# Kernel tuning notes

Measured on AMD Instinct MI355X. Metric: run time of the kernel, lower is better.

## Reference

```python
import jax, jax.numpy as jnp
import numpy as np

NEG_SLOPE = 0.2


def _gat_layer(x, W, a_src, a_dst, b, src, dst, n_nodes, heads, dim):
    # x: [N, F_in]; W: [F_in, heads*dim]
    h = (x @ W).reshape(n_nodes, heads, dim)            # [N,H,D]
    e_src = (h * a_src).sum(-1)                          # [N,H]
    e_dst = (h * a_dst).sum(-1)                          # [N,H]
    e = jax.nn.leaky_relu(e_src[src] + e_dst[dst], NEG_SLOPE)  # [E,H]
    # edge softmax over incoming edges of each target node
    m = jax.ops.segment_max(e, dst, num_segments=n_nodes)      # [N,H]
    ex = jnp.exp(e - m[dst])
    denom = jax.ops.segment_sum(ex, dst, num_segments=n_nodes)  # [N,H]
    alpha = ex / denom[dst]                              # [E,H]
    out = jax.ops.segment_sum(h[src] * alpha[:, :, None], dst,
                              num_segments=n_nodes)      # [N,H,D]
    return out.reshape(n_nodes, heads * dim) + b


def setup_inputs() -> dict:
    key = jax.random.key(0)
    ks = jax.random.split(key, 10)
    N, E, F_in = 100000, 1600000, 300
    x = jax.random.normal(ks[0], (N, F_in), dtype=jnp.float32)
    edge_index = jax.random.randint(ks[1], (2, E), 0, N, dtype=jnp.int64)
    s = 0.1
    return {
        'x': x,
        'edge_index': edge_index,
        'W1': jax.random.normal(ks[2], (F_in, 64), jnp.float32) * s,
        'att_src1': jax.random.normal(ks[3], (8, 8), jnp.float32) * s,
        'att_dst1': jax.random.normal(ks[4], (8, 8), jnp.float32) * s,
        'b1': jax.random.normal(ks[5], (64,), jnp.float32) * s,
        'W2': jax.random.normal(ks[6], (64, 64), jnp.float32) * s,
        'att_src2': jax.random.normal(ks[7], (1, 64), jnp.float32) * s,
        'att_dst2': jax.random.normal(ks[8], (1, 64), jnp.float32) * s,
        'b2': jax.random.normal(ks[9], (64,), jnp.float32) * s,
    }


def reference(x, edge_index, W1, att_src1, att_dst1, b1, W2, att_src2, att_dst2, b2):
    N = x.shape[0]
    # add self-loops (PyG GATConv default)
    loop = jnp.arange(N, dtype=edge_index.dtype)
    src = jnp.concatenate([edge_index[0], loop])
    dst = jnp.concatenate([edge_index[1], loop])
    # dropout p=0.6 is identity in eval mode
    h = _gat_layer(x, W1, att_src1, att_dst1, b1, src, dst, N, 8, 8)    # [N,64]
    h = jax.nn.elu(h)
    h = _gat_layer(h, W2, att_src2, att_dst2, b2, src, dst, N, 1, 64)   # [N,64]
    return jax.nn.log_softmax(h, axis=1)
```

## Files before the change

### kernel.cpp

```cpp
#include <hip/hip_runtime.h>
#include <math.h>

using short8 = __attribute__((ext_vector_type(8))) short;
using f32x4  = __attribute__((ext_vector_type(4))) float;

#define NBLKS 512
#define BPAD  800

__device__ __forceinline__ unsigned short f2bf(float f) {
    unsigned u = __float_as_uint(f);
    unsigned r = u + 0x7FFF + ((u >> 16) & 1);
    return (unsigned short)(r >> 16);
}


__global__ void detect64_kernel(const int* __restrict__ ei, int E, int* __restrict__ flag) {
    __shared__ int any;
    if (threadIdx.x == 0) any = 0;
    __syncthreads();
    for (int i = threadIdx.x; i < 1024; i += 256) {
        if (ei[2 * i + 1] != 0) { any = 1; break; }
    }
    __syncthreads();
    if (threadIdx.x == 0) *flag = (any ? 0 : 1);
}


__global__ __launch_bounds__(256) void binA_kernel(
    const int* __restrict__ ei, int E, int N, const int* __restrict__ flag,
    int nbuck, int* __restrict__ hist, int chunk) {
    __shared__ int lh[BPAD];
    for (int i = threadIdx.x; i < nbuck; i += 256) lh[i] = 0;
    __syncthreads();
    int is64 = *flag;
    int Etot = E + N;
    int beg = blockIdx.x * chunk, end = min(Etot, beg + chunk);
    for (int i = beg + threadIdx.x; i < end; i += 256) {
        int d = (i < E) ? (is64 ? ei[2 * (E + i)] : ei[E + i]) : (i - E);
        atomicAdd(&lh[d >> 7], 1);
    }
    __syncthreads();
    for (int i = threadIdx.x; i < nbuck; i += 256) hist[blockIdx.x * BPAD + i] = lh[i];
}

__global__ void scanBlocks_kernel(int* __restrict__ hist, int nbuck, int* __restrict__ bucketTotal) {
    int bin = blockIdx.x * 256 + threadIdx.x;
    if (bin >= nbuck) return;
    int run = 0;
    for (int b = 0; b < NBLKS; b++) {
        int v = hist[b * BPAD + bin];
        hist[b * BPAD + bin] = run;
        run += v;
    }
    bucketTotal[bin] = run;
}

__global__ void scanBucket_kernel(const int* __restrict__ bucketTotal, int nbuck,
                                  int* __restrict__ bucketBase) {
    __shared__ int s[1024];
    int t = threadIdx.x;
    int v = (t < nbuck) ? bucketTotal[t] : 0;
    s[t] = v;
    __syncthreads();
    for (int off = 1; off < 1024; off <<= 1) {
        int x = (t >= off) ? s[t - off] : 0;
        __syncthreads();
        s[t] += x;
        __syncthreads();
    }
    if (t < nbuck) bucketBase[t] = s[t] - v;
    if (t == nbuck - 1) bucketBase[nbuck] = s[t];
}

__global__ __launch_bounds__(256) void binB_kernel(
    const int* __restrict__ ei, int E, int N, const int* __restrict__ flag,
    int nbuck, const int* __restrict__ hist, const int* __restrict__ bucketBase,
    int* __restrict__ tmp, int chunk) {
    __shared__ int cur[BPAD];
    for (int i = threadIdx.x; i < nbuck; i += 256)
        cur[i] = bucketBase[i] + hist[blockIdx.x * BPAD + i];
    __syncthreads();
    int is64 = *flag;
    int Etot = E + N;
    int beg = blockIdx.x * chunk, end = min(Etot, beg + chunk);
    for (int i = beg + threadIdx.x; i < end; i += 256) {
        int s, d;
        if (i < E) {
            if (is64) { s = ei[2 * i]; d = ei[2 * (E + i)]; }
            else      { s = ei[i];     d = ei[E + i]; }
        } else { s = i - E; d = i - E; }
        int pos = atomicAdd(&cur[d >> 7], 1);
        tmp[pos] = ((d & 127) << 17) | s;
    }
}

__global__ __launch_bounds__(256) void binC_kernel(
    const int* __restrict__ tmp, const int* __restrict__ bucketBase, int nbuck,
    int N, int Etot, int* __restrict__ rowptr, int* __restrict__ col) {
    __shared__ int lh[128];
    __shared__ int cur[128];
    int g = blockIdx.x;
    int t = threadIdx.x;
    int beg = bucketBase[g], end = bucketBase[g + 1];
    if (t < 128) lh[t] = 0;
    __syncthreads();
    for (int i = beg + t; i < end; i += 256) atomicAdd(&lh[tmp[i] >> 17], 1);
    __syncthreads();
    int c = (t < 128) ? lh[t] : 0;
    for (int off = 1; off < 128; off <<= 1) {
        int x = 0;
        if (t < 128 && t >= off) x = lh[t - off];
        __syncthreads();
        if (t < 128) lh[t] += x;
        __syncthreads();
    }
    if (t < 128) {
        int excl = lh[t] - c;
        cur[t] = beg + excl;
        int node = g * 128 + t;
        if (node < N) rowptr[node] = beg + excl;
    }
    if (g == 0 && t == 0) rowptr[N] = Etot;
    __syncthreads();
    for (int i = beg + t; i < end; i += 256) {
        int v = tmp[i];
        int pos = atomicAdd(&cur[v >> 17], 1);
        col[pos] = v & 0x1FFFF;
    }
}


__global__ __launch_bounds__(256) void gemm1_mfma_kernel(
    const float* __restrict__ x, const float* __restrict__ W,
    const float* __restrict__ asrc, const float* __restrict__ adst,
    float* __restrict__ h, float* __restrict__ es, float* __restrict__ ed, int N) {
    __shared__ __align__(16) unsigned short A_lds[128 * 40];
    __shared__ __align__(16) unsigned short B_lds[64 * 40];
    const int tx = threadIdx.x;
    const int wv = tx >> 6;
    const int lane = tx & 63;
    const int l15 = lane & 15;
    const int quad = lane >> 4;
    const int rowBase = blockIdx.x * 128;

    f32x4 acc[2][4];
#pragma unroll
    for (int rt = 0; rt < 2; rt++)
#pragma unroll
        for (int ct = 0; ct < 4; ct++) acc[rt][ct] = (f32x4){0.f, 0.f, 0.f, 0.f};

    const int kq = tx & 7;
    const int r0 = tx >> 3;
    const int colB = tx & 63;
    const int kkb = (tx >> 6) * 8;

    for (int k0 = 0; k0 < 320; k0 += 32) {
        bool kvalid = (k0 + kq * 4 + 4 <= 300);
#pragma unroll
        for (int p = 0; p < 4; p++) {
            int row = p * 32 + r0;
            int grow = rowBase + row;
            float4 v = make_float4(0.f, 0.f, 0.f, 0.f);
            if (kvalid && grow < N) v = *(const float4*)&x[(size_t)grow * 300 + k0 + kq * 4];
            *(ushort4*)&A_lds[row * 40 + kq * 4] =
                make_ushort4(f2bf(v.x), f2bf(v.y), f2bf(v.z), f2bf(v.w));
        }
        {
            unsigned short t0, t1, t2, t3, t4, t5, t6, t7;
            float v;
            v = (k0 + kkb + 0 < 300) ? W[(size_t)(k0 + kkb + 0) * 64 + colB] : 0.f; t0 = f2bf(v);
            v = (k0 + kkb + 1 < 300) ? W[(size_t)(k0 + kkb + 1) * 64 + colB] : 0.f; t1 = f2bf(v);
            v = (k0 + kkb + 2 < 300) ? W[(size_t)(k0 + kkb + 2) * 64 + colB] : 0.f; t2 = f2bf(v);
            v = (k0 + kkb + 3 < 300) ? W[(size_t)(k0 + kkb + 3) * 64 + colB] : 0.f; t3 = f2bf(v);
            v = (k0 + kkb + 4 < 300) ? W[(size_t)(k0 + kkb + 4) * 64 + colB] : 0.f; t4 = f2bf(v);
            v = (k0 + kkb + 5 < 300) ? W[(size_t)(k0 + kkb + 5) * 64 + colB] : 0.f; t5 = f2bf(v);
            v = (k0 + kkb + 6 < 300) ? W[(size_t)(k0 + kkb + 6) * 64 + colB] : 0.f; t6 = f2bf(v);
            v = (k0 + kkb + 7 < 300) ? W[(size_t)(k0 + kkb + 7) * 64 + colB] : 0.f; t7 = f2bf(v);
            *(ushort4*)&B_lds[colB * 40 + kkb]     = make_ushort4(t0, t1, t2, t3);
            *(ushort4*)&B_lds[colB * 40 + kkb + 4] = make_ushort4(t4, t5, t6, t7);
        }
        __syncthreads();
        short8 af[2], bfr[4];
#pragma unroll
        for (int rt = 0; rt < 2; rt++)
            af[rt] = *(const short8*)&A_lds[(wv * 32 + rt * 16 + l15) * 40 + quad * 8];
#pragma unroll
        for (int ct = 0; ct < 4; ct++)
            bfr[ct] = *(const short8*)&B_lds[(ct * 16 + l15) * 40 + quad * 8];
#pragma unroll
        for (int rt = 0; rt < 2; rt++)
#pragma unroll
            for (int ct = 0; ct < 4; ct++)
                acc[rt][ct] = __builtin_amdgcn_mfma_f32_16x16x32_bf16(af[rt], bfr[ct], acc[rt][ct], 0, 0, 0);
        __syncthreads();
    }

    float as_v[4], ad_v[4];
#pragma unroll
    for (int ct = 0; ct < 4; ct++) {
        as_v[ct] = asrc[ct * 16 + l15];
        ad_v[ct] = adst[ct * 16 + l15];
    }
#pragma unroll
    for (int rt = 0; rt < 2; rt++) {
#pragma unroll
        for (int reg = 0; reg < 4; reg++) {
            int row = rowBase + wv * 32 + rt * 16 + quad * 4 + reg;
            bool ok = (row < N);
#pragma unroll
            for (int ct = 0; ct < 4; ct++) {
                float v = acc[rt][ct][reg];
                if (ok) h[(size_t)row * 64 + ct * 16 + l15] = v;
                float ps = v * as_v[ct];
                float pd = v * ad_v[ct];
                ps += __shfl_xor(ps, 1); ps += __shfl_xor(ps, 2); ps += __shfl_xor(ps, 4);
                pd += __shfl_xor(pd, 1); pd += __shfl_xor(pd, 2); pd += __shfl_xor(pd, 4);
                if ((lane & 7) == 0 && ok) {
                    int head = 2 * ct + ((lane >> 3) & 1);
                    es[row * 8 + head] = ps;
                    ed[row * 8 + head] = pd;
                }
            }
        }
    }
}


__global__ __launch_bounds__(256) void gemm2_kernel(
    const float* __restrict__ xin, const float* __restrict__ W,
    const float* __restrict__ asrc, const float* __restrict__ adst,
    float* __restrict__ h, float* __restrict__ es, float* __restrict__ ed, int N) {
    __shared__ __align__(16) float Ws[64 * 64];
    __shared__ float xs[128 * 65];
    const int tx = threadIdx.x;
    const int cg = tx & 7;
    const int rg = tx >> 3;
    const int rowBase = blockIdx.x * 128;
    float acc[4][8];
#pragma unroll
    for (int r = 0; r < 4; r++)
#pragma unroll
        for (int c = 0; c < 8; c++) acc[r][c] = 0.f;

    for (int i = tx; i < 64 * 64; i += 256) Ws[i] = W[i];
    for (int i = tx; i < 128 * 64; i += 256) {
        int rr = i >> 6, cc = i & 63;
        int row = rowBase + rr;
        xs[rr * 65 + cc] = (row < N) ? xin[(size_t)row * 64 + cc] : 0.f;
    }
    __syncthreads();
    for (int k = 0; k < 64; k++) {
        float4 w0 = *(const float4*)&Ws[k * 64 + cg * 8];
        float4 w1 = *(const float4*)&Ws[k * 64 + cg * 8 + 4];
#pragma unroll
        for (int r = 0; r < 4; r++) {
            float xv = xs[(rg * 4 + r) * 65 + k];
            acc[r][0] = fmaf(xv, w0.x, acc[r][0]);
            acc[r][1] = fmaf(xv, w0.y, acc[r][1]);
            acc[r][2] = fmaf(xv, w0.z, acc[r][2]);
            acc[r][3] = fmaf(xv, w0.w, acc[r][3]);
            acc[r][4] = fmaf(xv, w1.x, acc[r][4]);
            acc[r][5] = fmaf(xv, w1.y, acc[r][5]);
            acc[r][6] = fmaf(xv, w1.z, acc[r][6]);
            acc[r][7] = fmaf(xv, w1.w, acc[r][7]);
        }
    }
#pragma unroll
    for (int r = 0; r < 4; r++) {
        int row = rowBase + rg * 4 + r;
        float ps = 0.f, pd = 0.f;
        if (row < N) {
            float4 o0 = make_float4(acc[r][0], acc[r][1], acc[r][2], acc[r][3]);
            float4 o1 = make_float4(acc[r][4], acc[r][5], acc[r][6], acc[r][7]);
            *(float4*)&h[(size_t)row * 64 + cg * 8] = o0;
            *(float4*)&h[(size_t)row * 64 + cg * 8 + 4] = o1;
#pragma unroll
            for (int c = 0; c < 8; c++) {
                ps = fmaf(acc[r][c], asrc[cg * 8 + c], ps);
                pd = fmaf(acc[r][c], adst[cg * 8 + c], pd);
            }
        }
        for (int off = 1; off < 8; off <<= 1) {
            ps += __shfl_xor(ps, off);
            pd += __shfl_xor(pd, off);
        }
        if (cg == 0 && row < N) { es[row] = ps; ed[row] = pd; }
    }
}


#define EB 8
__global__ __launch_bounds__(256) void agg1_kernel(
    const int* __restrict__ rowptr, const int* __restrict__ col,
    const float* __restrict__ h, const float* __restrict__ es, const float* __restrict__ ed,
    const float* __restrict__ b, float* __restrict__ out, int N) {
    int node = blockIdx.x * 4 + (threadIdx.x >> 6);
    int lane = threadIdx.x & 63;
    if (node >= N) return;
    int hh = lane >> 3;
    float edv = ed[node * 8 + hh];
    float m = -1e30f, l = 0.f, acc = 0.f;
    int beg = rowptr[node], end = rowptr[node + 1];
    for (int i = beg; i < end; i += EB) {
        int ss[EB];
#pragma unroll
        for (int j = 0; j < EB; j++) {
            int idx = i + j;
            ss[j] = col[idx < end ? idx : end - 1];
        }
        float ev[EB], hv[EB];
#pragma unroll
        for (int j = 0; j < EB; j++) ev[j] = es[ss[j] * 8 + hh];
#pragma unroll
        for (int j = 0; j < EB; j++) hv[j] = h[(size_t)ss[j] * 64 + lane];
#pragma unroll
        for (int j = 0; j < EB; j++) {
            float e = ev[j] + edv;
            e = (e > 0.f) ? e : 0.2f * e;
            ev[j] = (i + j < end) ? e : -1e30f;
        }
        float mx = m;
#pragma unroll
        for (int j = 0; j < EB; j++) mx = fmaxf(mx, ev[j]);
        float sc = __expf(m - mx);
        float wsum = 0.f, asum = 0.f;
#pragma unroll
        for (int j = 0; j < EB; j++) {
            float wj = __expf(ev[j] - mx);
            wsum += wj;
            asum = fmaf(wj, hv[j], asum);
        }
        acc = fmaf(acc, sc, asum);
        l = fmaf(l, sc, wsum);
        m = mx;
    }
    float o = acc / l + b[lane];
    o = (o > 0.f) ? o : expm1f(o);
    out[(size_t)node * 64 + lane] = o;
}


__global__ __launch_bounds__(256) void agg2_kernel(
    const int* __restrict__ rowptr, const int* __restrict__ col,
    const float* __restrict__ h, const float* __restrict__ es, const float* __restrict__ ed,
    const float* __restrict__ b, float* __restrict__ out, int N) {
    int node = blockIdx.x * 4 + (threadIdx.x >> 6);
    int lane = threadIdx.x & 63;
    if (node >= N) return;
    float edv = ed[node];
    float m = -1e30f, l = 0.f, acc = 0.f;
    int beg = rowptr[node], end = rowptr[node + 1];
    for (int i = beg; i < end; i += EB) {
        int ss[EB];
#pragma unroll
        for (int j = 0; j < EB; j++) {
            int idx = i + j;
            ss[j] = col[idx < end ? idx : end - 1];
        }
        float ev[EB], hv[EB];
#pragma unroll
        for (int j = 0; j < EB; j++) ev[j] = es[ss[j]];
#pragma unroll
        for (int j = 0; j < EB; j++) hv[j] = h[(size_t)ss[j] * 64 + lane];
#pragma unroll
        for (int j = 0; j < EB; j++) {
            float e = ev[j] + edv;
            e = (e > 0.f) ? e : 0.2f * e;
            ev[j] = (i + j < end) ? e : -1e30f;
        }
        float mx = m;
#pragma unroll
        for (int j = 0; j < EB; j++) mx = fmaxf(mx, ev[j]);
        float sc = __expf(m - mx);
        float wsum = 0.f, asum = 0.f;
#pragma unroll
        for (int j = 0; j < EB; j++) {
            float wj = __expf(ev[j] - mx);
            wsum += wj;
            asum = fmaf(wj, hv[j], asum);
        }
        acc = fmaf(acc, sc, asum);
        l = fmaf(l, sc, wsum);
        m = mx;
    }
    float o = acc / l + b[lane];
    float M = o;
    for (int off = 32; off > 0; off >>= 1) M = fmaxf(M, __shfl_xor(M, off));
    float se = __expf(o - M);
    for (int off = 32; off > 0; off >>= 1) se += __shfl_xor(se, off);
    out[(size_t)node * 64 + lane] = o - M - logf(se);
}


extern "C" void kernel_launch(void* const* d_in, const int* in_sizes, int n_in,
                              void* d_out, int out_size, void* d_ws, size_t ws_size,
                              hipStream_t stream) {
    const float* x   = (const float*)d_in[0];
    const int*   ei  = (const int*)d_in[1];
    const float* W1  = (const float*)d_in[2];
    const float* as1 = (const float*)d_in[3];
    const float* ad1 = (const float*)d_in[4];
    const float* b1  = (const float*)d_in[5];
    const float* W2  = (const float*)d_in[6];
    const float* as2 = (const float*)d_in[7];
    const float* ad2 = (const float*)d_in[8];
    const float* b2  = (const float*)d_in[9];
    const int N = in_sizes[0] / 300;
    const int E = in_sizes[1] / 2;
    const int Etot = E + N;
    const int nbuck = (N + 127) >> 7;
    (void)n_in; (void)out_size; (void)ws_size;

    char* w = (char*)d_ws;
    auto alloc = [&](size_t bytes) -> char* {
        char* p = w;
        w += (bytes + 255) & ~(size_t)255;
        return p;
    };
    int*   flag        = (int*)alloc(256);
    int*   hist        = (int*)alloc((size_t)NBLKS * BPAD * 4);
    int*   bucketTotal = (int*)alloc((size_t)(BPAD + 1) * 4);
    int*   bucketBase  = (int*)alloc((size_t)(BPAD + 1) * 4);
    int*   tmp         = (int*)alloc((size_t)Etot * 4);
    int*   rowptr      = (int*)alloc((size_t)(N + 1) * 4);
    int*   col         = (int*)alloc((size_t)Etot * 4);
    float* h1          = (float*)alloc((size_t)N * 64 * 4);
    float* h1p         = (float*)alloc((size_t)N * 64 * 4);
    float* es1         = (float*)alloc((size_t)N * 8 * 4);
    float* ed1         = (float*)alloc((size_t)N * 8 * 4);
    float* es2         = (float*)alloc((size_t)N * 4);
    float* ed2         = (float*)alloc((size_t)N * 4);
    float* h2 = h1;

    detect64_kernel<<<1, 256, 0, stream>>>(ei, E, flag);

    int chunk = (Etot + NBLKS - 1) / NBLKS;
    binA_kernel<<<NBLKS, 256, 0, stream>>>(ei, E, N, flag, nbuck, hist, chunk);
    scanBlocks_kernel<<<(nbuck + 255) / 256, 256, 0, stream>>>(hist, nbuck, bucketTotal);
    scanBucket_kernel<<<1, 1024, 0, stream>>>(bucketTotal, nbuck, bucketBase);
    binB_kernel<<<NBLKS, 256, 0, stream>>>(ei, E, N, flag, nbuck, hist, bucketBase, tmp, chunk);
    binC_kernel<<<nbuck, 256, 0, stream>>>(tmp, bucketBase, nbuck, N, Etot, rowptr, col);

    gemm1_mfma_kernel<<<(N + 127) / 128, 256, 0, stream>>>(x, W1, as1, ad1, h1, es1, ed1, N);
    agg1_kernel<<<(N + 3) / 4, 256, 0, stream>>>(rowptr, col, h1, es1, ed1, b1, h1p, N);
    gemm2_kernel<<<(N + 127) / 128, 256, 0, stream>>>(h1p, W2, as2, ad2, h2, es2, ed2, N);
    agg2_kernel<<<(N + 3) / 4, 256, 0, stream>>>(rowptr, col, h2, es2, ed2, b2, (float*)d_out, N);
}
```

Measured before the change: 511.0 us.

## Precompute edge softmax weights in separate passes and port gemm2 to bf16 MFMA

Splits each aggregation into an alpha pass, where one thread per node/head computes the max and the exp weights and stores them per edge (bf16 for layer 1, fp32 for layer 2) along with the reciprocal denominator. The aggregation kernels then do a plain weighted sum with no online-softmax rescaling. gemm2 is also rewritten to use bf16 MFMA instead of scalar FMA, and col is padded so the tail loads need no clamping. The alpha pass re-reads es over edges twice, serially per thread, and adds an extra per-edge weight stream, while bf16 weights and inputs reduce precision.

```diff
diff --git a/kernel.cpp b/kernel.cpp
--- a/kernel.cpp
+++ b/kernel.cpp
@@ -6,6 +6,7 @@
 
 #define NBLKS 512
 #define BPAD  800
+#define EB 8
 
 __device__ __forceinline__ unsigned short f2bf(float f) {
     unsigned u = __float_as_uint(f);
@@ -121,6 +122,7 @@
         if (node < N) rowptr[node] = beg + excl;
     }
     if (g == 0 && t == 0) rowptr[N] = Etot;
+    if (g == 0 && t < 8) col[Etot + t] = 0;
     __syncthreads();
     for (int i = beg + t; i < end; i += 256) {
         int v = tmp[i];
@@ -226,164 +228,205 @@
 }
 
 
-__global__ __launch_bounds__(256) void gemm2_kernel(
+__global__ __launch_bounds__(256) void gemm2_mfma_kernel(
     const float* __restrict__ xin, const float* __restrict__ W,
     const float* __restrict__ asrc, const float* __restrict__ adst,
     float* __restrict__ h, float* __restrict__ es, float* __restrict__ ed, int N) {
-    __shared__ __align__(16) float Ws[64 * 64];
-    __shared__ float xs[128 * 65];
+    __shared__ __align__(16) unsigned short A_lds[128 * 72];
+    __shared__ __align__(16) unsigned short B_lds[64 * 72];
     const int tx = threadIdx.x;
-    const int cg = tx & 7;
-    const int rg = tx >> 3;
+    const int wv = tx >> 6;
+    const int lane = tx & 63;
+    const int l15 = lane & 15;
+    const int quad = lane >> 4;
     const int rowBase = blockIdx.x * 128;
-    float acc[4][8];
-#pragma unroll
-    for (int r = 0; r < 4; r++)
-#pragma unroll
-        for (int c = 0; c < 8; c++) acc[r][c] = 0.f;
-
-    for (int i = tx; i < 64 * 64; i += 256) Ws[i] = W[i];
-    for (int i = tx; i < 128 * 64; i += 256) {
-        int rr = i >> 6, cc = i & 63;
-        int row = rowBase + rr;
-        xs[rr * 65 + cc] = (row < N) ? xin[(size_t)row * 64 + cc] : 0.f;
-    }
-    __syncthreads();
-    for (int k = 0; k < 64; k++) {
-        float4 w0 = *(const float4*)&Ws[k * 64 + cg * 8];
-        float4 w1 = *(const float4*)&Ws[k * 64 + cg * 8 + 4];
-#pragma unroll
-        for (int r = 0; r < 4; r++) {
-            float xv = xs[(rg * 4 + r) * 65 + k];
-            acc[r][0] = fmaf(xv, w0.x, acc[r][0]);
-            acc[r][1] = fmaf(xv, w0.y, acc[r][1]);
-            acc[r][2] = fmaf(xv, w0.z, acc[r][2]);
-            acc[r][3] = fmaf(xv, w0.w, acc[r][3]);
-            acc[r][4] = fmaf(xv, w1.x, acc[r][4]);
-            acc[r][5] = fmaf(xv, w1.y, acc[r][5]);
-            acc[r][6] = fmaf(xv, w1.z, acc[r][6]);
-            acc[r][7] = fmaf(xv, w1.w, acc[r][7]);
-        }
-    }
-#pragma unroll
-    for (int r = 0; r < 4; r++) {
-        int row = rowBase + rg * 4 + r;
-        float ps = 0.f, pd = 0.f;
-        if (row < N) {
-            float4 o0 = make_float4(acc[r][0], acc[r][1], acc[r][2], acc[r][3]);
-            float4 o1 = make_float4(acc[r][4], acc[r][5], acc[r][6], acc[r][7]);
-            *(float4*)&h[(size_t)row * 64 + cg * 8] = o0;
-            *(float4*)&h[(size_t)row * 64 + cg * 8 + 4] = o1;
-#pragma unroll
-            for (int c = 0; c < 8; c++) {
-                ps = fmaf(acc[r][c], asrc[cg * 8 + c], ps);
-                pd = fmaf(acc[r][c], adst[cg * 8 + c], pd);
+
+    f32x4 acc[2][4];
+#pragma unroll
+    for (int rt = 0; rt < 2; rt++)
+#pragma unroll
+        for (int ct = 0; ct < 4; ct++) acc[rt][ct] = (f32x4){0.f, 0.f, 0.f, 0.f};
+
+    {
+        int colB = tx & 63;
+        int kk = (tx >> 6) * 16;
+#pragma unroll
+        for (int j = 0; j < 16; j++)
+            B_lds[colB * 72 + kk + j] = f2bf(W[(size_t)(kk + j) * 64 + colB]);
+    }
+    {
+        int kq = tx & 15, r0 = tx >> 4;
+#pragma unroll
+        for (int p = 0; p < 8; p++) {
+            int row = p * 16 + r0;
+            int grow = rowBase + row;
+            float4 v = make_float4(0.f, 0.f, 0.f, 0.f);
+            if (grow < N) v = *(const float4*)&xin[(size_t)grow * 64 + kq * 4];
+            *(ushort4*)&A_lds[row * 72 + kq * 4] =
+                make_ushort4(f2bf(v.x), f2bf(v.y), f2bf(v.z), f2bf(v.w));
+        }
+    }
+    __syncthreads();
+#pragma unroll
+    for (int c = 0; c < 2; c++) {
+        short8 af[2], bfr[4];
+#pragma unroll
+        for (int rt = 0; rt < 2; rt++)
+            af[rt] = *(const short8*)&A_lds[(wv * 32 + rt * 16 + l15) * 72 + quad * 8 + c * 32];
+#pragma unroll
+        for (int ct = 0; ct < 4; ct++)
+            bfr[ct] = *(const short8*)&B_lds[(ct * 16 + l15) * 72 + quad * 8 + c * 32];
+#pragma unroll
+        for (int rt = 0; rt < 2; rt++)
+#pragma unroll
+            for (int ct = 0; ct < 4; ct++)
+                acc[rt][ct] = __builtin_amdgcn_mfma_f32_16x16x32_bf16(af[rt], bfr[ct], acc[rt][ct], 0, 0, 0);
+    }
+
+    float as_v[4], ad_v[4];
+#pragma unroll
+    for (int ct = 0; ct < 4; ct++) {
+        as_v[ct] = asrc[ct * 16 + l15];
+        ad_v[ct] = adst[ct * 16 + l15];
+    }
+#pragma unroll
+    for (int rt = 0; rt < 2; rt++) {
+#pragma unroll
+        for (int reg = 0; reg < 4; reg++) {
+            int row = rowBase + wv * 32 + rt * 16 + quad * 4 + reg;
+            bool ok = (row < N);
+            float ps = 0.f, pd = 0.f;
+#pragma unroll
+            for (int ct = 0; ct < 4; ct++) {
+                float v = acc[rt][ct][reg];
+                if (ok) h[(size_t)row * 64 + ct * 16 + l15] = v;
+                ps = fmaf(v, as_v[ct], ps);
+                pd = fmaf(v, ad_v[ct], pd);
             }
-        }
-        for (int off = 1; off < 8; off <<= 1) {
-            ps += __shfl_xor(ps, off);
-            pd += __shfl_xor(pd, off);
-        }
-        if (cg == 0 && row < N) { es[row] = ps; ed[row] = pd; }
-    }
-}
-
-
-#define EB 8
-__global__ __launch_bounds__(256) void agg1_kernel(
+            ps += __shfl_xor(ps, 1); ps += __shfl_xor(ps, 2);
+            ps += __shfl_xor(ps, 4); ps += __shfl_xor(ps, 8);
+            pd += __shfl_xor(pd, 1); pd += __shfl_xor(pd, 2);
+            pd += __shfl_xor(pd, 4); pd += __shfl_xor(pd, 8);
+            if (l15 == 0 && ok) { es[row] = ps; ed[row] = pd; }
+        }
+    }
+}
+
+
+__global__ __launch_bounds__(256) void alpha1_kernel(
     const int* __restrict__ rowptr, const int* __restrict__ col,
-    const float* __restrict__ h, const float* __restrict__ es, const float* __restrict__ ed,
-    const float* __restrict__ b, float* __restrict__ out, int N) {
+    const float* __restrict__ es, const float* __restrict__ ed,
+    unsigned short* __restrict__ w1a, float* __restrict__ rden, int N) {
+    int tid = blockIdx.x * 256 + threadIdx.x;
+    int node = tid >> 3, head = tid & 7;
+    if (node >= N) return;
+    int beg = rowptr[node], end = rowptr[node + 1];
+    float edv = ed[node * 8 + head];
+    float m = -1e30f;
+    for (int e = beg; e < end; e++) {
+        int s = col[e];
+        float v = es[s * 8 + head] + edv;
+        v = (v > 0.f) ? v : 0.2f * v;
+        m = fmaxf(m, v);
+    }
+    float l = 0.f;
+    for (int e = beg; e < end; e++) {
+        int s = col[e];
+        float v = es[s * 8 + head] + edv;
+        v = (v > 0.f) ? v : 0.2f * v;
+        float wj = __expf(v - m);
+        l += wj;
+        w1a[e * 8 + head] = f2bf(wj);
+    }
+    rden[node * 8 + head] = 1.f / l;
+}
+
+__global__ __launch_bounds__(256) void alpha2_kernel(
+    const int* __restrict__ rowptr, const int* __restrict__ col,
+    const float* __restrict__ es, const float* __restrict__ ed,
+    float* __restrict__ w2a, float* __restrict__ rden, int N) {
+    int node = blockIdx.x * 256 + threadIdx.x;
+    if (node >= N) return;
+    int beg = rowptr[node], end = rowptr[node + 1];
+    float edv = ed[node];
+    float m = -1e30f;
+    for (int e = beg; e < end; e++) {
+        float v = es[col[e]] + edv;
+        v = (v > 0.f) ? v : 0.2f * v;
+        m = fmaxf(m, v);
+    }
+    float l = 0.f;
+    for (int e = beg; e < end; e++) {
+        float v = es[col[e]] + edv;
+        v = (v > 0.f) ? v : 0.2f * v;
+        float wj = __expf(v - m);
+        l += wj;
+        w2a[e] = wj;
+    }
+    rden[node] = 1.f / l;
+}
+
+
+__global__ __launch_bounds__(256) void agg1g_kernel(
+    const int* __restrict__ rowptr, const int* __restrict__ col,
+    const float* __restrict__ h, const unsigned short* __restrict__ w1a,
+    const float* __restrict__ rden, const float* __restrict__ b,
+    float* __restrict__ out, int N) {
     int node = blockIdx.x * 4 + (threadIdx.x >> 6);
     int lane = threadIdx.x & 63;
     if (node >= N) return;
     int hh = lane >> 3;
-    float edv = ed[node * 8 + hh];
-    float m = -1e30f, l = 0.f, acc = 0.f;
     int beg = rowptr[node], end = rowptr[node + 1];
+    float rinv = rden[node * 8 + hh];
+    float acc = 0.f;
     for (int i = beg; i < end; i += EB) {
         int ss[EB];
+        float wv[EB], hv[EB];
+#pragma unroll
+        for (int j = 0; j < EB; j++) ss[j] = col[i + j];
 #pragma unroll
         for (int j = 0; j < EB; j++) {
-            int idx = i + j;
-            ss[j] = col[idx < end ? idx : end - 1];
-        }
-        float ev[EB], hv[EB];
-#pragma unroll
-        for (int j = 0; j < EB; j++) ev[j] = es[ss[j] * 8 + hh];
+            unsigned wr = w1a[(i + j) * 8 + hh];
+            wv[j] = __uint_as_float(wr << 16);
+        }
 #pragma unroll
         for (int j = 0; j < EB; j++) hv[j] = h[(size_t)ss[j] * 64 + lane];
 #pragma unroll
-        for (int j = 0; j < EB; j++) {
-            float e = ev[j] + edv;
-            e = (e > 0.f) ? e : 0.2f * e;
-            ev[j] = (i + j < end) ? e : -1e30f;
-        }
-        float mx = m;
-#pragma unroll
-        for (int j = 0; j < EB; j++) mx = fmaxf(mx, ev[j]);
-        float sc = __expf(m - mx);
-        float wsum = 0.f, asum = 0.f;
-#pragma unroll
-        for (int j = 0; j < EB; j++) {
-            float wj = __expf(ev[j] - mx);
-            wsum += wj;
-            asum = fmaf(wj, hv[j], asum);
-        }
-        acc = fmaf(acc, sc, asum);
-        l = fmaf(l, sc, wsum);
-        m = mx;
-    }
-    float o = acc / l + b[lane];
+        for (int j = 0; j < EB; j++) wv[j] = (i + j < end) ? wv[j] : 0.f;
+#pragma unroll
+        for (int j = 0; j < EB; j++) acc = fmaf(wv[j], hv[j], acc);
+    }
+    float o = acc * rinv + b[lane];
     o = (o > 0.f) ? o : expm1f(o);
     out[(size_t)node * 64 + lane] = o;
 }
 
-
-__global__ __launch_bounds__(256) void agg2_kernel(
+__global__ __launch_bounds__(256) void agg2g_kernel(
     const int* __restrict__ rowptr, const int* __restrict__ col,
-    const float* __restrict__ h, const float* __restrict__ es, const float* __restrict__ ed,
-    const float* __restrict__ b, float* __restrict__ out, int N) {
+    const float* __restrict__ h, const float* __restrict__ w2a,
+    const float* __restrict__ rden, const float* __restrict__ b,
+    float* __restrict__ out, int N) {
     int node = blockIdx.x * 4 + (threadIdx.x >> 6);
     int lane = threadIdx.x & 63;
     if (node >= N) return;
-    float edv = ed[node];
-    float m = -1e30f, l = 0.f, acc = 0.f;
     int beg = rowptr[node], end = rowptr[node + 1];
+    float rinv = rden[node];
+    float acc = 0.f;
     for (int i = beg; i < end; i += EB) {
         int ss[EB];
-#pragma unroll
-        for (int j = 0; j < EB; j++) {
-            int idx = i + j;
-            ss[j] = col[idx < end ? idx : end - 1];
-        }
-        float ev[EB], hv[EB];
-#pragma unroll
-        for (int j = 0; j < EB; j++) ev[j] = es[ss[j]];
+        float wv[EB], hv[EB];
+#pragma unroll
+        for (int j = 0; j < EB; j++) ss[j] = col[i + j];
+#pragma unroll
+        for (int j = 0; j < EB; j++) wv[j] = w2a[i + j];
 #pragma unroll
         for (int j = 0; j < EB; j++) hv[j] = h[(size_t)ss[j] * 64 + lane];
 #pragma unroll
-        for (int j = 0; j < EB; j++) {
-            float e = ev[j] + edv;
-            e = (e > 0.f) ? e : 0.2f * e;
-            ev[j] = (i + j < end) ? e : -1e30f;
-        }
-        float mx = m;
-#pragma unroll
-        for (int j = 0; j < EB; j++) mx = fmaxf(mx, ev[j]);
-        float sc = __expf(m - mx);
-        float wsum = 0.f, asum = 0.f;
-#pragma unroll
-        for (int j = 0; j < EB; j++) {
-            float wj = __expf(ev[j] - mx);
-            wsum += wj;
-            asum = fmaf(wj, hv[j], asum);
-        }
-        acc = fmaf(acc, sc, asum);
-        l = fmaf(l, sc, wsum);
-        m = mx;
-    }
-    float o = acc / l + b[lane];
+        for (int j = 0; j < EB; j++) wv[j] = (i + j < end) ? wv[j] : 0.f;
+#pragma unroll
+        for (int j = 0; j < EB; j++) acc = fmaf(wv[j], hv[j], acc);
+    }
+    float o = acc * rinv + b[lane];
     float M = o;
     for (int off = 32; off > 0; off >>= 1) M = fmaxf(M, __shfl_xor(M, off));
     float se = __expf(o - M);
@@ -421,16 +464,20 @@
     int*   hist        = (int*)alloc((size_t)NBLKS * BPAD * 4);
     int*   bucketTotal = (int*)alloc((size_t)(BPAD + 1) * 4);
     int*   bucketBase  = (int*)alloc((size_t)(BPAD + 1) * 4);
-    int*   tmp         = (int*)alloc((size_t)Etot * 4);
+    int*   tmp         = (int*)alloc((size_t)(Etot + 8) * 4);
     int*   rowptr      = (int*)alloc((size_t)(N + 1) * 4);
-    int*   col         = (int*)alloc((size_t)Etot * 4);
+    int*   col         = (int*)alloc((size_t)(Etot + 8) * 4);
     float* h1          = (float*)alloc((size_t)N * 64 * 4);
     float* h1p         = (float*)alloc((size_t)N * 64 * 4);
     float* es1         = (float*)alloc((size_t)N * 8 * 4);
     float* ed1         = (float*)alloc((size_t)N * 8 * 4);
     float* es2         = (float*)alloc((size_t)N * 4);
     float* ed2         = (float*)alloc((size_t)N * 4);
+    unsigned short* w1a = (unsigned short*)alloc((size_t)(Etot + 8) * 8 * 2);
+    float* rden1       = (float*)alloc((size_t)N * 8 * 4);
+    float* rden2       = (float*)alloc((size_t)N * 4);
     float* h2 = h1;
+    float* w2a = (float*)tmp;
 
     detect64_kernel<<<1, 256, 0, stream>>>(ei, E, flag);
 
@@ -442,7 +489,9 @@
     binC_kernel<<<nbuck, 256, 0, stream>>>(tmp, bucketBase, nbuck, N, Etot, rowptr, col);
 
     gemm1_mfma_kernel<<<(N + 127) / 128, 256, 0, stream>>>(x, W1, as1, ad1, h1, es1, ed1, N);
-    agg1_kernel<<<(N + 3) / 4, 256, 0, stream>>>(rowptr, col, h1, es1, ed1, b1, h1p, N);
-    gemm2_kernel<<<(N + 127) / 128, 256, 0, stream>>>(h1p, W2, as2, ad2, h2, es2, ed2, N);
-    agg2_kernel<<<(N + 3) / 4, 256, 0, stream>>>(rowptr, col, h2, es2, ed2, b2, (float*)d_out, N);
-}
+    alpha1_kernel<<<(N * 8 + 255) / 256, 256, 0, stream>>>(rowptr, col, es1, ed1, w1a, rden1, N);
+    agg1g_kernel<<<(N + 3) / 4, 256, 0, stream>>>(rowptr, col, h1, w1a, rden1, b1, h1p, N);
+    gemm2_mfma_kernel<<<(N + 127) / 128, 256, 0, stream>>>(h1p, W2, as2, ad2, h2, es2, ed2, N);
+    alpha2_kernel<<<(N + 255) / 256, 256, 0, stream>>>(rowptr, col, es2, ed2, w2a, rden2, N);
+    agg2g_kernel<<<(N + 3) / 4, 256, 0, stream>>>(rowptr, col, h2, w2a, rden2, b2, (float*)d_out, N);
+}
```

New measurement: 545.7 us. +6.8%, slower.
